# Performance work log

Measured on AMD Instinct MI355X. Metric: run time of the kernel, lower is better.

Reference implementation:

```python
import jax, jax.numpy as jnp
import numpy as np

N = 16384
D = 128
TOPK = 32


def setup_inputs() -> dict:
    key = jax.random.key(0)
    kx, kw = jax.random.split(key)
    x = jax.random.normal(kx, (N,), dtype=jnp.float32)  # unused by the module's forward
    W = jax.random.normal(kw, (N, D), dtype=jnp.float32)  # embedding table (learned param)
    return {"x": x, "W": W}


def reference(x, W):
    # adj = E @ E^T : [N, N] similarity matrix
    adj = W @ W.T
    # per-row top-K (torch.topk along dim=1)
    vals, idx = jax.lax.top_k(adj, TOPK)  # [N, K] each
    # dense_to_sparse emits nonzeros in row-major order -> sort columns within each row.
    order = jnp.argsort(idx, axis=1)
    idx_s = jnp.take_along_axis(idx, order, axis=1)
    vals_s = jnp.take_along_axis(vals, order, axis=1)
    rows = jnp.repeat(jnp.arange(N, dtype=idx_s.dtype), TOPK)
    edge_index = jnp.stack([rows, idx_s.reshape(-1)])  # [2, N*K]
    edge_values = vals_s.reshape(-1)  # [N*K]
    return edge_index, edge_values
```

## Files before the change

### kernel.cpp

```cpp
#include <hip/hip_runtime.h>
#include <hip/hip_bf16.h>
#include <hip/hip_fp16.h>


#define N_ROWS 16384
#define DIM    128
#define TOPK   32
#define NK     (N_ROWS * TOPK)
#define ZTAU   2.45f
#define DELTA  0.05f
#define NSEG   8
#define SEGCAP 48
#define CAPB   16
#define WCAP   48
#define NWAVE  8
#define TILE   256
#define NT     (N_ROWS / TILE)
#define NPAIR  (NT * (NT + 1) / 2)
#define W1BIN  0.15625f
#define W2BIN  0.00244140625f

using short8   = __attribute__((ext_vector_type(8)))  short;
using floatx16 = __attribute__((ext_vector_type(16))) float;

#define PK_ROWS 32
__global__ __launch_bounds__(256)
void pack_kernel(const float* __restrict__ W, unsigned short* __restrict__ F,
                 float* __restrict__ norm, float* __restrict__ tau,
                 unsigned int* __restrict__ gcnt) {
    __shared__ float lds[PK_ROWS * 132];
    __shared__ float nrmS[PK_ROWS];
    const int t  = threadIdx.x;
    const int rb = blockIdx.x * PK_ROWS;

    { const int gid = blockIdx.x * 256 + t;
      gcnt[gid] = 0u; }

    const float4* src = (const float4*)(W + (size_t)rb * DIM);
    #pragma unroll
    for (int i = 0; i < 4; ++i) {
        const int f = t + 256 * i;
        const float4 v = src[f];
        const int r = f >> 5, j = f & 31;
        *(float4*)&lds[r * 132 + j * 4] = v;
        float ss = v.x * v.x + v.y * v.y + v.z * v.z + v.w * v.w;
        #pragma unroll
        for (int off = 1; off < 32; off <<= 1) ss += __shfl_xor(ss, off, 64);
        if (j == 0) nrmS[r] = sqrtf(ss);
    }
    __syncthreads();

    const size_t blkoff = (size_t)blockIdx.x * 8192;
    uint2* fb = (uint2*)((char*)F + blkoff);
    #pragma unroll
    for (int i = 0; i < 4; ++i) {
        const int p   = t + 256 * i;
        const int D   = 2 * p;
        const int q   = D >> 7, r31 = (D >> 2) & 31, w = D & 3;
        const float4 f4 = *(const float4*)&lds[r31 * 132 + q * 8 + w * 2];
        __hip_bfloat16 b0 = __float2bfloat16(f4.x), b1 = __float2bfloat16(f4.y);
        __hip_bfloat16 b2 = __float2bfloat16(f4.z), b3 = __float2bfloat16(f4.w);
        fb[p] = make_uint2(
            (unsigned)(*(unsigned short*)&b0) | ((unsigned)(*(unsigned short*)&b1) << 16),
            (unsigned)(*(unsigned short*)&b2) | ((unsigned)(*(unsigned short*)&b3) << 16));
    }
    if (t < PK_ROWS) { norm[rb + t] = nrmS[t]; tau[rb + t] = ZTAU * nrmS[t]; }
}

__global__ __launch_bounds__(512, 4)
void score_kernel(const unsigned short* __restrict__ F,
                  const float* __restrict__ tau,
                  unsigned int* __restrict__ gcnt,
                  unsigned int* __restrict__ gcand) {
    __shared__ unsigned short Bs[128 * DIM];
    __shared__ unsigned int   lcand[512 * CAPB];
    __shared__ unsigned int   lcnt[512];

    const int tid = threadIdx.x, lane = tid & 63, wid = tid >> 6;
    const int half = lane >> 5, l31 = lane & 31;
    const unsigned seg = (unsigned)(blockIdx.x & (NSEG - 1));

    int ti = 0, rem = blockIdx.x;
    while (rem >= NT - ti) { rem -= NT - ti; ++ti; }
    const int tj = ti + rem;
    const int Rbase = ti * TILE, Cbase = tj * TILE;
    const bool offdiag = (ti != tj);

    lcnt[tid] = 0u;

    short8 afrag[8];
    {
        const char* ab = (const char*)F + (size_t)((Rbase >> 5) + wid) * 8192
                       + half * 512 + l31 * 16;
        #pragma unroll
        for (int k = 0; k < 8; ++k) afrag[k] = *(const short8*)(ab + k * 1024);
    }
    float rt[16];
    #pragma unroll
    for (int r = 0; r < 16; ++r)
        rt[r] = tau[Rbase + wid * 32 + 4 * half + (r & 3) + 8 * (r >> 2)];

    #pragma unroll 1
    for (int ph = 0; ph < 2; ++ph) {
        __syncthreads();
        {
            const short8* src = (const short8*)((const char*)F
                              + ((size_t)(Cbase >> 5) + 4 * ph) * 8192);
            short8* dst = (short8*)Bs;
            #pragma unroll
            for (int c = 0; c < 4; ++c) dst[tid + 512 * c] = src[tid + 512 * c];
        }
        __syncthreads();

        #pragma unroll 1
        for (int cb = 0; cb < 4; ++cb) {
            const int colbase = Cbase + ph * 128 + cb * 32;
            const int col = colbase + l31;
            const float ctv = offdiag ? tau[col] : 3.0e38f;

            short8 bf[8];
            const char* bb = (const char*)Bs + cb * 8192 + half * 512 + l31 * 16;
            #pragma unroll
            for (int k = 0; k < 8; ++k) bf[k] = *(const short8*)(bb + k * 1024);

            floatx16 acc = (floatx16)0.0f;
            #pragma unroll
            for (int k = 0; k < 8; ++k)
                acc = __builtin_amdgcn_mfma_f32_32x32x16_bf16(afrag[k], bf[k], acc, 0, 0, 0);

            #pragma unroll
            for (int r = 0; r < 16; ++r) {
                const float raw = acc[r];
                if (raw > fminf(rt[r], ctv)) {
                    const int lrow = wid * 32 + 4 * half + (r & 3) + 8 * (r >> 2);
                    const unsigned short h = __half_as_ushort(__float2half(raw));
                    if (raw > rt[r]) {
                        unsigned slot = atomicAdd(&lcnt[lrow], 1u);
                        if (slot < CAPB)
                            lcand[lrow * CAPB + slot] = ((unsigned)col << 16) | h;
                    }
                    if (raw > ctv) {
                        const int lcol = 256 + ph * 128 + cb * 32 + l31;
                        const unsigned grow = (unsigned)(Rbase + lrow);
                        unsigned slot = atomicAdd(&lcnt[lcol], 1u);
                        if (slot < CAPB)
                            lcand[lcol * CAPB + slot] = (grow << 16) | h;
                    }
                }
            }
        }
    }
    __syncthreads();

    int c = (int)lcnt[tid]; if (c > CAPB) c = CAPB;
    if (c > 0) {
        const int grow = (tid < 256) ? (Rbase + tid) : (Cbase + (tid - 256));
        const unsigned base = atomicAdd(&gcnt[(size_t)seg * N_ROWS + grow], (unsigned)c);
        unsigned int* dst = &gcand[((size_t)grow * NSEG + seg) * SEGCAP];
        for (int i = 0; i < c; ++i) {
            const unsigned slot = base + i;
            if (slot < SEGCAP) dst[slot] = lcand[tid * CAPB + i];
        }
    }
}

__global__ __launch_bounds__(512)
void tail_kernel(const unsigned int* __restrict__ gcnt,
                 const unsigned int* __restrict__ gcand,
                 const float* __restrict__ W, const float* __restrict__ norm,
                 float* __restrict__ out) {
    __shared__ unsigned int candS[NWAVE][NSEG * SEGCAP];
    __shared__ int          wcolS[NWAVE][WCAP];
    __shared__ double       dvalS[NWAVE][WCAP];
    __shared__ int          fcolS[NWAVE][TOPK];
    __shared__ float        fvalS[NWAVE][TOPK];
    __shared__ unsigned int wcntS[NWAVE], mcntS[NWAVE], fcntS[NWAVE];

    const int tid = threadIdx.x, lane = tid & 63, wid = tid >> 6;
    const int rowg = blockIdx.x * NWAVE + wid;
    const float inv = 1.0f / norm[rowg];

    int cs[NSEG];
    #pragma unroll
    for (int s = 0; s < NSEG; ++s) {
        int c = (int)gcnt[(size_t)s * N_ROWS + rowg];
        cs[s] = c > SEGCAP ? SEGCAP : c;
    }
    int n = 0;
    #pragma unroll
    for (int s = 0; s < NSEG; ++s) {
        const unsigned int* src = gcand + ((size_t)rowg * NSEG + s) * SEGCAP;
        for (int i = lane; i < cs[s]; i += 64) candS[wid][n + i] = src[i];
        n += cs[s];
    }
    const unsigned int* cl = &candS[wid][0];

    unsigned int* histW = (unsigned int*)&dvalS[wid][0];

    if (lane == 0) { wcntS[wid] = 0u; mcntS[wid] = 0u; fcntS[wid] = 0u; }
    histW[lane] = 0u;
    for (int i = lane; i < n; i += 64) {
        const float v = __half2float(__ushort_as_half((unsigned short)(cl[i] & 0xFFFFu))) * inv;
        int b = (int)((v - ZTAU) * (1.0f / W1BIN));
        b = b < 0 ? 0 : (b > 63 ? 63 : b);
        atomicAdd(&histW[b], 1u);
    }
    unsigned sfx = histW[lane];
    #pragma unroll
    for (int off = 1; off < 64; off <<= 1) {
        unsigned u = __shfl_down(sfx, off, 64);
        if (lane + off < 64) sfx += u;
    }
    unsigned long long mk = __ballot(sfx >= (unsigned)TOPK);
    const int b1 = mk ? (63 - __clzll(mk)) : 0;
    unsigned Gup = __shfl(sfx, (b1 + 1) & 63, 64);
    if (b1 == 63) Gup = 0u;
    const float lo1 = ZTAU + (float)b1 * W1BIN;

    histW[lane] = 0u;
    for (int i = lane; i < n; i += 64) {
        const float v = __half2float(__ushort_as_half((unsigned short)(cl[i] & 0xFFFFu))) * inv;
        if (v >= lo1 && v < lo1 + W1BIN) {
            int b = (int)((v - lo1) * (1.0f / W2BIN));
            b = b < 0 ? 0 : (b > 63 ? 63 : b);
            atomicAdd(&histW[b], 1u);
        }
    }
    unsigned sfx2 = histW[lane];
    #pragma unroll
    for (int off = 1; off < 64; off <<= 1) {
        unsigned u = __shfl_down(sfx2, off, 64);
        if (lane + off < 64) sfx2 += u;
    }
    sfx2 += Gup;
    mk = __ballot(sfx2 >= (unsigned)TOPK);
    const int b2 = mk ? (63 - __clzll(mk)) : 0;
    const float vlo = lo1 + (float)b2 * W2BIN;
    const float vhi = vlo + W2BIN;

    for (int i = lane; i < n; i += 64) {
        const unsigned e = cl[i];
        const float v = __half2float(__ushort_as_half((unsigned short)(e & 0xFFFFu))) * inv;
        if (v > vhi + DELTA) {
            atomicAdd(&mcntS[wid], 1u);
        } else if (v >= vlo - DELTA) {
            unsigned u = atomicAdd(&wcntS[wid], 1u);
            if (u < WCAP) wcolS[wid][u] = (int)(e >> 16);
        }
    }
    const int m = (int)mcntS[wid];
    int wn = (int)wcntS[wid]; if (wn > WCAP) wn = WCAP;
    int need = TOPK - m; if (need < 0) need = 0;

    if (lane < wn) {
        const int col = wcolS[wid][lane] & (N_ROWS - 1);
        const float4* wa = (const float4*)(W + (size_t)rowg * DIM);
        const float4* wb = (const float4*)(W + (size_t)col * DIM);
        double d0 = 0, d1 = 0, d2 = 0, d3 = 0;
        #pragma unroll
        for (int k = 0; k < DIM / 4; ++k) {
            const float4 x = wa[k]; const float4 y = wb[k];
            d0 += (double)x.x * y.x; d1 += (double)x.y * y.y;
            d2 += (double)x.z * y.z; d3 += (double)x.w * y.w;
        }
        dvalS[wid][lane] = (d0 + d1) + (d2 + d3);
    }
    if (lane < wn) {
        const double dv = dvalS[wid][lane]; const int c = wcolS[wid][lane];
        int r = 0;
        for (int u = 0; u < wn; ++u) {
            const double du = dvalS[wid][u];
            r += (du > dv || (du == dv && wcolS[wid][u] < c)) ? 1 : 0;
        }
        if (r < need) {
            unsigned slot = atomicAdd(&fcntS[wid], 1u);
            if (slot < TOPK) { fcolS[wid][slot] = c; fvalS[wid][slot] = (float)dv; }
        }
    }
    for (int i = lane; i < n; i += 64) {
        const unsigned e = cl[i];
        const float vr = __half2float(__ushort_as_half((unsigned short)(e & 0xFFFFu)));
        if (vr * inv > vhi + DELTA) {
            unsigned slot = atomicAdd(&fcntS[wid], 1u);
            if (slot < TOPK) { fcolS[wid][slot] = (int)(e >> 16); fvalS[wid][slot] = vr; }
        }
    }
    int fn = (int)fcntS[wid]; if (fn > TOPK) fn = TOPK;
    if (lane < fn) {
        const int c = fcolS[wid][lane];
        int pos = 0;
        for (int j = 0; j < fn; ++j) pos += (fcolS[wid][j] < c) ? 1 : 0;
        const size_t base = (size_t)rowg * TOPK + pos;
        out[base]                  = (float)rowg;
        out[NK + base]             = (float)c;
        out[2 * (size_t)NK + base] = fvalS[wid][lane];
    }
}

extern "C" void kernel_launch(void* const* d_in, const int* in_sizes, int n_in,
                              void* d_out, int out_size, void* d_ws, size_t ws_size,
                              hipStream_t stream) {
    (void)in_sizes; (void)n_in; (void)out_size; (void)ws_size;
    const float* W   = (const float*)d_in[1];
    float*       out = (float*)d_out;

    char* ws = (char*)d_ws;
    unsigned short* F    = (unsigned short*)ws;
    float*          norm = (float*)(ws + (size_t)4194304);
    float*          tau  = (float*)(ws + (size_t)4259840);
    unsigned int*   gcnt = (unsigned int*)(ws + (size_t)4325376);
    unsigned int*   gcand= (unsigned int*)(ws + (size_t)4849664);

    pack_kernel<<<N_ROWS / PK_ROWS, 256, 0, stream>>>(W, F, norm, tau, gcnt);
    score_kernel<<<NPAIR, 512, 0, stream>>>(F, tau, gcnt, gcand);
    tail_kernel<<<N_ROWS / NWAVE, 512, 0, stream>>>(gcnt, gcand, W, norm, out);
}
```

Before: 209.9 us.

## Shrink per-block candidate buffer, spill overflow to global, prefetch B tiles in registers

Cuts the per-row LDS candidate capacity in half and sends overflow candidates straight to the global segmented buffer via global atomics, so fewer candidates are silently dropped. This shrinks LDS use so the launch bound can be raised from 4 to 6 blocks per CU. The B-tile loads now go through registers, with the second phase's tile fetched while the first is being stored to LDS, to hide global load latency. The risks are more global atomics when rows overflow the smaller local buffer, and extra register pressure under the tighter launch bound.

```diff
diff --git a/kernel.cpp b/kernel.cpp
--- a/kernel.cpp
+++ b/kernel.cpp
@@ -11,7 +11,7 @@
 #define DELTA  0.05f
 #define NSEG   8
 #define SEGCAP 48
-#define CAPB   16
+#define CAPB   8
 #define WCAP   48
 #define NWAVE  8
 #define TILE   256
@@ -67,7 +67,7 @@
     if (t < PK_ROWS) { norm[rb + t] = nrmS[t]; tau[rb + t] = ZTAU * nrmS[t]; }
 }
 
-__global__ __launch_bounds__(512, 4)
+__global__ __launch_bounds__(512, 6)
 void score_kernel(const unsigned short* __restrict__ F,
                   const float* __restrict__ tau,
                   unsigned int* __restrict__ gcnt,
@@ -88,6 +88,13 @@
 
     lcnt[tid] = 0u;
 
+    short8 st0, st1, st2, st3;
+    {
+        const short8* src = (const short8*)((const char*)F + (size_t)(Cbase >> 5) * 8192);
+        st0 = src[tid];  st1 = src[tid + 512];
+        st2 = src[tid + 1024]; st3 = src[tid + 1536];
+    }
+
     short8 afrag[8];
     {
         const char* ab = (const char*)F + (size_t)((Rbase >> 5) + wid) * 8192
@@ -100,22 +107,27 @@
     for (int r = 0; r < 16; ++r)
         rt[r] = tau[Rbase + wid * 32 + 4 * half + (r & 3) + 8 * (r >> 2)];
 
+    unsigned int* cntSeg = gcnt + (size_t)seg * N_ROWS;
+
     #pragma unroll 1
     for (int ph = 0; ph < 2; ++ph) {
         __syncthreads();
         {
+            short8* dst = (short8*)Bs;
+            dst[tid]        = st0;  dst[tid + 512]  = st1;
+            dst[tid + 1024] = st2;  dst[tid + 1536] = st3;
+        }
+        if (ph == 0) {
             const short8* src = (const short8*)((const char*)F
-                              + ((size_t)(Cbase >> 5) + 4 * ph) * 8192);
-            short8* dst = (short8*)Bs;
-            #pragma unroll
-            for (int c = 0; c < 4; ++c) dst[tid + 512 * c] = src[tid + 512 * c];
+                              + ((size_t)(Cbase >> 5) + 4) * 8192);
+            st0 = src[tid];  st1 = src[tid + 512];
+            st2 = src[tid + 1024]; st3 = src[tid + 1536];
         }
         __syncthreads();
 
         #pragma unroll 1
         for (int cb = 0; cb < 4; ++cb) {
-            const int colbase = Cbase + ph * 128 + cb * 32;
-            const int col = colbase + l31;
+            const int col = Cbase + ph * 128 + cb * 32 + l31;
             const float ctv = offdiag ? tau[col] : 3.0e38f;
 
             short8 bf[8];
@@ -135,16 +147,29 @@
                     const int lrow = wid * 32 + 4 * half + (r & 3) + 8 * (r >> 2);
                     const unsigned short h = __half_as_ushort(__float2half(raw));
                     if (raw > rt[r]) {
+                        const unsigned e = ((unsigned)col << 16) | h;
                         unsigned slot = atomicAdd(&lcnt[lrow], 1u);
-                        if (slot < CAPB)
-                            lcand[lrow * CAPB + slot] = ((unsigned)col << 16) | h;
+                        if (slot < CAPB) {
+                            lcand[lrow * CAPB + slot] = e;
+                        } else {
+                            const int grow = Rbase + lrow;
+                            unsigned g = atomicAdd(&cntSeg[grow], 1u);
+                            if (g < SEGCAP)
+                                gcand[((size_t)grow * NSEG + seg) * SEGCAP + g] = e;
+                        }
                     }
                     if (raw > ctv) {
                         const int lcol = 256 + ph * 128 + cb * 32 + l31;
-                        const unsigned grow = (unsigned)(Rbase + lrow);
+                        const unsigned e = ((unsigned)(Rbase + lrow) << 16) | h;
                         unsigned slot = atomicAdd(&lcnt[lcol], 1u);
-                        if (slot < CAPB)
-                            lcand[lcol * CAPB + slot] = (grow << 16) | h;
+                        if (slot < CAPB) {
+                            lcand[lcol * CAPB + slot] = e;
+                        } else {
+                            const int grow = Cbase + (lcol - 256);
+                            unsigned g = atomicAdd(&cntSeg[grow], 1u);
+                            if (g < SEGCAP)
+                                gcand[((size_t)grow * NSEG + seg) * SEGCAP + g] = e;
+                        }
                     }
                 }
             }
@@ -155,7 +180,7 @@
     int c = (int)lcnt[tid]; if (c > CAPB) c = CAPB;
     if (c > 0) {
         const int grow = (tid < 256) ? (Rbase + tid) : (Cbase + (tid - 256));
-        const unsigned base = atomicAdd(&gcnt[(size_t)seg * N_ROWS + grow], (unsigned)c);
+        const unsigned base = atomicAdd(&cntSeg[grow], (unsigned)c);
         unsigned int* dst = &gcand[((size_t)grow * NSEG + seg) * SEGCAP];
         for (int i = 0; i < c; ++i) {
             const unsigned slot = base + i;
```

Result: slower. 438.1 us (+108.8%).
